# Optimization experiments

Measured on AMD Instinct MI355X. Metric: run time of the kernel, lower is better.

Reference implementation:

```python
import jax, jax.numpy as jnp
import numpy as np

# Problem sizes (see shape_source): 32 point clouds of 2048 points each.
B, P, K = 32, 2048, 20
DIN, H, OUT = 3, 128, 128
N = B * P
EPS = 1e-5  # BatchNorm eps (eval mode: running stats mean=0, var=1)


def setup_inputs() -> dict:
    key = jax.random.key(0)
    ks = jax.random.split(key, 8)
    x = jax.random.normal(ks[0], (N, DIN), dtype=jnp.float32)
    batch = (jnp.arange(N) // P).astype(jnp.int32)  # equal-size clouds

    def lin(k, i, o):
        return (jax.random.normal(k, (i, o), dtype=jnp.float32) / np.sqrt(i)).astype(jnp.float32)

    return {
        "x": x, "batch": batch,
        # transfer = MLP([input_dim, hid_dim]) -> single Linear
        "Wt": lin(ks[1], DIN, H), "bt": jnp.zeros((H,), jnp.float32),
        # GINConv layer 0: Linear(H,2H) -> ReLU -> Linear(2H,H)
        "W1_0": lin(ks[2], H, 2 * H), "b1_0": jnp.zeros((2 * H,), jnp.float32),
        "W2_0": lin(ks[3], 2 * H, H), "b2_0": jnp.zeros((H,), jnp.float32),
        "g0": jnp.ones((H,), jnp.float32), "be0": jnp.zeros((H,), jnp.float32),
        "rm0": jnp.zeros((H,), jnp.float32), "rv0": jnp.ones((H,), jnp.float32),
        # GINConv layer 1
        "W1_1": lin(ks[4], H, 2 * H), "b1_1": jnp.zeros((2 * H,), jnp.float32),
        "W2_1": lin(ks[5], 2 * H, OUT), "b2_1": jnp.zeros((OUT,), jnp.float32),
        "g1": jnp.ones((OUT,), jnp.float32), "be1": jnp.zeros((OUT,), jnp.float32),
        "rm1": jnp.zeros((OUT,), jnp.float32), "rv1": jnp.ones((OUT,), jnp.float32),
    }


def _knn_idx(x):
    """Per-cloud kNN (includes self, dist 0), returns global neighbor ids [N,K]."""
    xb = x.reshape(B, P, DIN)
    sq = jnp.sum(xb * xb, axis=-1)  # [B,P]
    # squared euclidean distance [B,P,P]
    dist = sq[:, :, None] + sq[:, None, :] - 2.0 * jnp.einsum('bpd,bqd->bpq', xb, xb)
    _, idx = jax.lax.top_k(-dist, K)  # [B,P,K] nearest (incl. self)
    offs = (jnp.arange(B, dtype=idx.dtype) * P)[:, None, None]
    return (idx + offs).reshape(N, K)


def _bn_eval(h, g, be, rm, rv):
    return g * (h - rm) * jax.lax.rsqrt(rv + EPS) + be


def _gin_max(h, nbr, W1, b1, W2, b2):
    # max-aggregation over kNN neighbors + self loop, then GIN MLP
    agg = jnp.maximum(jnp.max(h[nbr], axis=1), h)  # [N,d]
    return jax.nn.relu(agg @ W1 + b1) @ W2 + b2


def reference(x, batch, Wt, bt,
              W1_0, b1_0, W2_0, b2_0, g0, be0, rm0, rv0,
              W1_1, b1_1, W2_1, b2_1, g1, be1, rm1, rv1):
    nbr = _knn_idx(jax.lax.stop_gradient(x))  # knn(x, x, k, batch).flip([0])
    h = x @ Wt + bt  # transfer MLP (single Linear)
    # layer 0: GINConv(max) -> BN -> ReLU (dropout identity in eval)
    h = _gin_max(h, nbr, W1_0, b1_0, W2_0, b2_0)
    h = jax.nn.relu(_bn_eval(h, g0, be0, rm0, rv0))
    # layer 1 (last): GINConv(max) -> BN -> dropout (identity)
    h = _gin_max(h, nbr, W1_1, b1_1, W2_1, b2_1)
    h = _bn_eval(h, g1, be1, rm1, rv1)
    return h
```

## Files before the change

### kernel.cpp

```cpp
#include <hip/hip_runtime.h>

typedef unsigned int u32;
typedef unsigned short u16;
typedef unsigned long long u64;

#define NPTS 65536
#define PCLD 2048
#define KNN 20
#define HD 128
#define HD2 256

typedef __attribute__((ext_vector_type(8))) short bf16x8;
typedef __attribute__((ext_vector_type(4))) float f32x4;
typedef unsigned short us2 __attribute__((ext_vector_type(2)));

__device__ __forceinline__ u16 f2bf(float f) {
    u32 u = __float_as_uint(f);
    u32 r = (u + 0x7FFFu + ((u >> 16) & 1u)) >> 16;
    return (u16)r;
}
__device__ __forceinline__ u32 enc2(u32 b) {
    u32 s = (b >> 15) & 0x00010001u;
    return b ^ (s * 0x7FFFu) ^ 0x80008000u;
}
__device__ __forceinline__ u32 dec2(u32 e) {
    u32 s = ((~e) >> 15) & 0x00010001u;
    return e ^ (s * 0x7FFFu) ^ 0x80008000u;
}
__device__ __forceinline__ u32 max2(u32 a, u32 b) {
#if __has_builtin(__builtin_elementwise_max)
    us2 x, y; __builtin_memcpy(&x, &a, 4); __builtin_memcpy(&y, &b, 4);
    us2 r = __builtin_elementwise_max(x, y);
    u32 o; __builtin_memcpy(&o, &r, 4); return o;
#else
    u32 lo = ((a & 0xFFFFu) > (b & 0xFFFFu)) ? (a & 0xFFFFu) : (b & 0xFFFFu);
    u32 hi = ((a >> 16) > (b >> 16)) ? (a & 0xFFFF0000u) : (b & 0xFFFF0000u);
    return lo | hi;
#endif
}

__global__ __launch_bounds__(256) void prep_kernel(
    const float* __restrict__ W1_0, const float* __restrict__ W2_0,
    const float* __restrict__ W1_1, const float* __restrict__ W2_1,
    u16* __restrict__ W1_0T, u16* __restrict__ W2_0T,
    u16* __restrict__ W1_1T, u16* __restrict__ W2_1T) {
    int id = blockIdx.x * 256 + threadIdx.x;
    int m = id >> 15, e = id & 32767;
    if (m == 0)      { int n = e >> 7, k = e & 127; W1_0T[e] = f2bf(W1_0[k * 256 + n]); }
    else if (m == 1) { int n = e >> 8, k = e & 255; W2_0T[e] = f2bf(W2_0[k * 128 + n]); }
    else if (m == 2) { int n = e >> 7, k = e & 127; W1_1T[e] = f2bf(W1_1[k * 256 + n]); }
    else             { int n = e >> 8, k = e & 255; W2_1T[e] = f2bf(W2_1[k * 128 + n]); }
}

__global__ __launch_bounds__(256) void knn_kernel(const float* __restrict__ x,
                                                  u16* __restrict__ nbr) {
    __shared__ float4 pts[PCLD];
    const int cloud = blockIdx.x >> 3;
    const int qi = ((blockIdx.x & 7) << 8) + threadIdx.x;
    const float* xc = x + (u64)cloud * PCLD * 3;
    for (int t = threadIdx.x; t < PCLD; t += 256) {
        float a = xc[3 * t], b = xc[3 * t + 1], c = xc[3 * t + 2];
        float sq = __fadd_rn(__fadd_rn(__fmul_rn(a, a), __fmul_rn(b, b)), __fmul_rn(c, c));
        pts[t] = make_float4(a, b, c, sq);
    }
    __syncthreads();
    const float4 q = pts[qi];
    const float qx = q.x, qy = q.y, qz = q.z, qs = q.w;
    const int lane = threadIdx.x & 63;
    u64 list[KNN];
#pragma unroll
    for (int k = 0; k < KNN; ++k) list[k] = 0xFF800000FFFFFFFFull;
    float thr = __builtin_inff();

    for (int base = 0; base < PCLD; base += 64) {
        float4 cp = pts[base + lane];
        u64 mask = 0;
#pragma unroll
        for (int c = 0; c < 64; ++c) {
            float cx = __uint_as_float(__builtin_amdgcn_readlane(__float_as_uint(cp.x), c));
            float cy = __uint_as_float(__builtin_amdgcn_readlane(__float_as_uint(cp.y), c));
            float cz = __uint_as_float(__builtin_amdgcn_readlane(__float_as_uint(cp.z), c));
            float cs = __uint_as_float(__builtin_amdgcn_readlane(__float_as_uint(cp.w), c));
            float dot = __builtin_fmaf(cz, qz, __builtin_fmaf(cy, qy, __fmul_rn(cx, qx)));
            float d = __fsub_rn(__fadd_rn(qs, cs), __fmul_rn(2.0f, dot));
            if (d < thr) mask |= (1ull << c);
        }
        while (mask) {
            int c = __builtin_ctzll(mask);
            mask &= mask - 1;
            float4 p2 = pts[base + c];
            float dot = __builtin_fmaf(p2.z, qz, __builtin_fmaf(p2.y, qy, __fmul_rn(p2.x, qx)));
            float d = __fsub_rn(__fadd_rn(qs, p2.w), __fmul_rn(2.0f, dot));
            if (d < thr) {
                u32 ub = __float_as_uint(d);
                u32 e = (ub & 0x80000000u) ? ~ub : (ub | 0x80000000u);
                u64 key = (((u64)e) << 32) | (u32)(base + c);
#pragma unroll
                for (int k = 0; k < KNN; ++k) {
                    u64 lo = key < list[k] ? key : list[k];
                    u64 hi = key < list[k] ? list[k] : key;
                    list[k] = lo; key = hi;
                }
                u32 e19 = (u32)(list[KNN - 1] >> 32);
                u32 ud = (e19 & 0x80000000u) ? (e19 & 0x7FFFFFFFu) : ~e19;
                thr = __uint_as_float(ud);
            }
        }
    }
    u16* out = nbr + (u64)(cloud * PCLD + qi) * KNN;
#pragma unroll
    for (int k = 0; k < KNN; ++k) out[k] = (u16)(u32)list[k];
}

__global__ __launch_bounds__(256) void feat_kernel(const float* __restrict__ x,
                                                   const float* __restrict__ Wt,
                                                   const float* __restrict__ bt,
                                                   u16* __restrict__ h0e) {
    int gid = blockIdx.x * 256 + threadIdx.x;
    int i = gid >> 4;
    int g = gid & 15;
    int c0 = g << 3;
    float x0 = x[3 * i], x1 = x[3 * i + 1], x2 = x[3 * i + 2];
    u32 o[4];
#pragma unroll
    for (int j = 0; j < 8; j += 2) {
        int c = c0 + j;
        float a0 = bt[c]     + x0 * Wt[c]     + x1 * Wt[128 + c]     + x2 * Wt[256 + c];
        float a1 = bt[c + 1] + x0 * Wt[c + 1] + x1 * Wt[128 + c + 1] + x2 * Wt[256 + c + 1];
        o[j >> 1] = enc2(((u32)f2bf(a0)) | (((u32)f2bf(a1)) << 16));
    }
    uint4* dst = (uint4*)&h0e[(u64)g * NPTS * 8 + (u64)i * 8];
    *dst = make_uint4(o[0], o[1], o[2], o[3]);
}

__global__ __launch_bounds__(256) void agg_kernel(const u16* __restrict__ he,
                                                  const u16* __restrict__ nbr,
                                                  u16* __restrict__ agge) {
    __shared__ u16 hL[PCLD * 8];
    const int tid = threadIdx.x;
    const int cloud = blockIdx.x >> 4;
    const int s = blockIdx.x & 15;
    const u16* __restrict__ src = he + (u64)s * NPTS * 8 + (u64)cloud * PCLD * 8;

    for (int k = 0; k < 8; ++k) {
        int r = tid + 256 * k;
        *(uint4*)&hL[r * 8] = *(const uint4*)&src[(u64)r * 8];
    }
    __syncthreads();

    const int rowbase = cloud * PCLD;
    for (int k = 0; k < 8; ++k) {
        int r = tid + 256 * k;
        uint4 m = *(const uint4*)&hL[r * 8];
        const u64* nb8 = (const u64*)(nbr + (u64)(rowbase + r) * KNN);
        u64 nq[5];
#pragma unroll
        for (int w = 0; w < 5; ++w) nq[w] = nb8[w];
#pragma unroll
        for (int t = 0; t < KNN; ++t) {
            int loc = (int)(nq[t >> 2] >> ((t & 3) * 16)) & (PCLD - 1);
            uint4 v = *(const uint4*)&hL[loc * 8];
            m.x = max2(m.x, v.x); m.y = max2(m.y, v.y);
            m.z = max2(m.z, v.z); m.w = max2(m.w, v.w);
        }
        *(uint4*)&agge[(u64)s * NPTS * 8 + (u64)(rowbase + r) * 8] = m;
    }
}

template <int RELU_OUT, int OUT_F32>
__global__ __launch_bounds__(256) void gemm_kernel(
    const u16* __restrict__ agge,
    const u16* __restrict__ W1T, const float* __restrict__ b1,
    const u16* __restrict__ W2T, const float* __restrict__ b2,
    const float* __restrict__ g, const float* __restrict__ be,
    const float* __restrict__ rm, const float* __restrict__ rv,
    void* __restrict__ hout_v) {
    __shared__ u16 aggL[64][136];
    __shared__ u16 hidL[64][264];
    const int tid = threadIdx.x;
    const int R = blockIdx.x * 64;

    {
        const int r = tid >> 2, cg = tid & 3;
        const int gr = R + r;
#pragma unroll
        for (int h = 0; h < 4; ++h) {
            const int s = 4 * cg + h;
            const u32* src = (const u32*)(agge + (u64)s * NPTS * 8 + (u64)gr * 8);
            u32 w0 = src[0], w1 = src[1], w2 = src[2], w3 = src[3];
            u32* dst = (u32*)&aggL[r][cg * 32 + h * 8];
            dst[0] = dec2(w0); dst[1] = dec2(w1); dst[2] = dec2(w2); dst[3] = dec2(w3);
        }
    }
    __syncthreads();

    const int wv = tid >> 6, lane = tid & 63;
    const int lr = lane & 15;
    const int lq = lane >> 4;

    {
        f32x4 acc[4][4];
#pragma unroll
        for (int i = 0; i < 4; ++i)
#pragma unroll
            for (int j = 0; j < 4; ++j) acc[i][j] = (f32x4)(0.0f);
        const int nb0 = wv * 64;
#pragma unroll
        for (int ks = 0; ks < 4; ++ks) {
            const int kcol = ks * 32 + lq * 8;
            bf16x8 af[4], bfr[4];
#pragma unroll
            for (int mt = 0; mt < 4; ++mt)
                af[mt] = *(const bf16x8*)&aggL[mt * 16 + lr][kcol];
#pragma unroll
            for (int nt = 0; nt < 4; ++nt)
                bfr[nt] = *(const bf16x8*)&W1T[(u64)(nb0 + nt * 16 + lr) * HD + kcol];
#pragma unroll
            for (int mt = 0; mt < 4; ++mt)
#pragma unroll
                for (int nt = 0; nt < 4; ++nt)
                    acc[mt][nt] = __builtin_amdgcn_mfma_f32_16x16x32_bf16(af[mt], bfr[nt], acc[mt][nt], 0, 0, 0);
        }
#pragma unroll
        for (int nt = 0; nt < 4; ++nt) {
            const int c = nb0 + nt * 16 + lr;
            const float bias = b1[c];
#pragma unroll
            for (int mt = 0; mt < 4; ++mt)
#pragma unroll
                for (int r2 = 0; r2 < 4; ++r2) {
                    float v = fmaxf(acc[mt][nt][r2] + bias, 0.0f);
                    hidL[mt * 16 + lq * 4 + r2][c] = f2bf(v);
                }
        }
    }
    __syncthreads();

    {
        f32x4 acc[4][2];
#pragma unroll
        for (int i = 0; i < 4; ++i) { acc[i][0] = (f32x4)(0.0f); acc[i][1] = (f32x4)(0.0f); }
        const int nb0 = wv * 32;
#pragma unroll
        for (int ks = 0; ks < 8; ++ks) {
            const int kcol = ks * 32 + lq * 8;
            bf16x8 af[4], bfr[2];
#pragma unroll
            for (int mt = 0; mt < 4; ++mt)
                af[mt] = *(const bf16x8*)&hidL[mt * 16 + lr][kcol];
#pragma unroll
            for (int nt = 0; nt < 2; ++nt)
                bfr[nt] = *(const bf16x8*)&W2T[(u64)(nb0 + nt * 16 + lr) * HD2 + kcol];
#pragma unroll
            for (int mt = 0; mt < 4; ++mt)
#pragma unroll
                for (int nt = 0; nt < 2; ++nt)
                    acc[mt][nt] = __builtin_amdgcn_mfma_f32_16x16x32_bf16(af[mt], bfr[nt], acc[mt][nt], 0, 0, 0);
        }
#pragma unroll
        for (int nt = 0; nt < 2; ++nt) {
            const int c = nb0 + nt * 16 + lr;
            const float bias = b2[c];
            const float sc = g[c] * (1.0f / sqrtf(rv[c] + 1e-5f));
            const float rmc = rm[c];
            const float bec = be[c];
#pragma unroll
            for (int mt = 0; mt < 4; ++mt)
#pragma unroll
                for (int r2 = 0; r2 < 4; ++r2) {
                    float v = acc[mt][nt][r2] + bias;
                    v = (v - rmc) * sc + bec;
                    if (RELU_OUT) v = fmaxf(v, 0.0f);
                    const int row = R + mt * 16 + lq * 4 + r2;
                    if (OUT_F32) {
                        ((float*)hout_v)[(u64)row * HD + c] = v;
                    } else {
                        u16 b = f2bf(v);
                        u16 e = b ^ ((b & 0x8000u) ? (u16)0xFFFFu : (u16)0x8000u);
                        ((u16*)hout_v)[(u64)(c >> 3) * NPTS * 8 + (u64)row * 8 + (c & 7)] = e;
                    }
                }
        }
    }
}

extern "C" void kernel_launch(void* const* d_in, const int* in_sizes, int n_in,
                              void* d_out, int out_size, void* d_ws, size_t ws_size,
                              hipStream_t stream) {
    const float* x    = (const float*)d_in[0];
    const float* Wt   = (const float*)d_in[2];
    const float* bt   = (const float*)d_in[3];
    const float* W1_0 = (const float*)d_in[4];
    const float* b1_0 = (const float*)d_in[5];
    const float* W2_0 = (const float*)d_in[6];
    const float* b2_0 = (const float*)d_in[7];
    const float* g0   = (const float*)d_in[8];
    const float* be0  = (const float*)d_in[9];
    const float* rm0  = (const float*)d_in[10];
    const float* rv0  = (const float*)d_in[11];
    const float* W1_1 = (const float*)d_in[12];
    const float* b1_1 = (const float*)d_in[13];
    const float* W2_1 = (const float*)d_in[14];
    const float* b2_1 = (const float*)d_in[15];
    const float* g1   = (const float*)d_in[16];
    const float* be1  = (const float*)d_in[17];
    const float* rm1  = (const float*)d_in[18];
    const float* rv1  = (const float*)d_in[19];

    char* ws = (char*)d_ws;
    u16* he   = (u16*)ws;
    u16* agge = (u16*)(ws + 16777216);
    u16* W10T = (u16*)(ws + 2 * 16777216);
    u16* W20T = W10T + 32768;
    u16* W11T = W20T + 32768;
    u16* W21T = W11T + 32768;
    u16* nbr  = (u16*)(ws + 2 * 16777216 + 4 * 65536);

    knn_kernel<<<256, 256, 0, stream>>>(x, nbr);
    prep_kernel<<<512, 256, 0, stream>>>(W1_0, W2_0, W1_1, W2_1, W10T, W20T, W11T, W21T);
    feat_kernel<<<4096, 256, 0, stream>>>(x, Wt, bt, he);
    agg_kernel<<<512, 256, 0, stream>>>(he, nbr, agge);
    gemm_kernel<1, 0><<<1024, 256, 0, stream>>>(agge, W10T, b1_0, W20T, b2_0,
                                                g0, be0, rm0, rv0, he);
    agg_kernel<<<512, 256, 0, stream>>>(he, nbr, agge);
    gemm_kernel<0, 1><<<1024, 256, 0, stream>>>(agge, W11T, b1_1, W21T, b2_1,
                                                g1, be1, rm1, rv1, d_out);
}
```

Baseline: 344.2 us.

## Split kNN candidate scan across two thread halves and merge top-k lists

The kNN kernel now runs 512 threads per block. Each query is handled by two threads, and each thread scans half of the cloud's candidate points. The second half writes its sorted top-20 list to shared memory, and the first half merges it into its own list with an insertion network before writing the result. This doubles the number of active waves to expose more parallelism, since only 256 blocks were launched before. The cost is extra shared memory, a block barrier, a serial merge step, and weaker early thresholds in each half.

```diff
diff --git a/kernel.cpp b/kernel.cpp
--- a/kernel.cpp
+++ b/kernel.cpp
@@ -52,27 +52,31 @@
     else             { int n = e >> 8, k = e & 255; W2_1T[e] = f2bf(W2_1[k * 128 + n]); }
 }
 
-__global__ __launch_bounds__(256) void knn_kernel(const float* __restrict__ x,
+__global__ __launch_bounds__(512) void knn_kernel(const float* __restrict__ x,
                                                   u16* __restrict__ nbr) {
     __shared__ float4 pts[PCLD];
+    __shared__ u64 lists[KNN][256];
+    const int tid = threadIdx.x;
     const int cloud = blockIdx.x >> 3;
-    const int qi = ((blockIdx.x & 7) << 8) + threadIdx.x;
+    const int ql = ((blockIdx.x & 7) << 8) + (tid & 255);
+    const int half = tid >> 8;
     const float* xc = x + (u64)cloud * PCLD * 3;
-    for (int t = threadIdx.x; t < PCLD; t += 256) {
+    for (int t = tid; t < PCLD; t += 512) {
         float a = xc[3 * t], b = xc[3 * t + 1], c = xc[3 * t + 2];
         float sq = __fadd_rn(__fadd_rn(__fmul_rn(a, a), __fmul_rn(b, b)), __fmul_rn(c, c));
         pts[t] = make_float4(a, b, c, sq);
     }
     __syncthreads();
-    const float4 q = pts[qi];
+    const float4 q = pts[ql];
     const float qx = q.x, qy = q.y, qz = q.z, qs = q.w;
-    const int lane = threadIdx.x & 63;
+    const int lane = tid & 63;
     u64 list[KNN];
 #pragma unroll
     for (int k = 0; k < KNN; ++k) list[k] = 0xFF800000FFFFFFFFull;
     float thr = __builtin_inff();
 
-    for (int base = 0; base < PCLD; base += 64) {
+    const int cbeg = half << 10;
+    for (int base = cbeg; base < cbeg + 1024; base += 64) {
         float4 cp = pts[base + lane];
         u64 mask = 0;
 #pragma unroll
@@ -107,9 +111,27 @@
             }
         }
     }
-    u16* out = nbr + (u64)(cloud * PCLD + qi) * KNN;
-#pragma unroll
-    for (int k = 0; k < KNN; ++k) out[k] = (u16)(u32)list[k];
+
+    if (half) {
+#pragma unroll
+        for (int k = 0; k < KNN; ++k) lists[k][tid & 255] = list[k];
+    }
+    __syncthreads();
+    if (!half) {
+#pragma unroll
+        for (int j = 0; j < KNN; ++j) {
+            u64 key = lists[j][tid];
+#pragma unroll
+            for (int k = 0; k < KNN; ++k) {
+                u64 lo = key < list[k] ? key : list[k];
+                u64 hi = key < list[k] ? list[k] : key;
+                list[k] = lo; key = hi;
+            }
+        }
+        u16* out = nbr + (u64)(cloud * PCLD + ql) * KNN;
+#pragma unroll
+        for (int k = 0; k < KNN; ++k) out[k] = (u16)(u32)list[k];
+    }
 }
 
 __global__ __launch_bounds__(256) void feat_kernel(const float* __restrict__ x,
@@ -316,7 +338,7 @@
     u16* W21T = W11T + 32768;
     u16* nbr  = (u16*)(ws + 2 * 16777216 + 4 * 65536);
 
-    knn_kernel<<<256, 256, 0, stream>>>(x, nbr);
+    knn_kernel<<<256, 512, 0, stream>>>(x, nbr);
     prep_kernel<<<512, 256, 0, stream>>>(W1_0, W2_0, W1_1, W2_1, W10T, W20T, W11T, W21T);
     feat_kernel<<<4096, 256, 0, stream>>>(x, Wt, bt, he);
     agg_kernel<<<512, 256, 0, stream>>>(he, nbr, agge);
```

Measured after the change: 399.1 us. 1.16x slower.

## Fuse neighbor max-aggregation into GEMM kernel with row-major features

Applied to the files above, without the earlier changes.

Removes the separate LDS-based aggregation kernel and performs the kNN max-gather directly inside the GEMM kernel's tile load, reading neighbor rows from global memory in a row-major feature layout. Blocks are remapped so tiles of the same cloud land on the same XCD, aiming for L2 reuse of the cloud's features. This eliminates the agge round-trip and two launches, but replaces LDS gathers with scattered global gathers of 64-byte row chunks.

```diff
diff --git a/kernel.cpp b/kernel.cpp
--- a/kernel.cpp
+++ b/kernel.cpp
@@ -129,47 +129,13 @@
         float a1 = bt[c + 1] + x0 * Wt[c + 1] + x1 * Wt[128 + c + 1] + x2 * Wt[256 + c + 1];
         o[j >> 1] = enc2(((u32)f2bf(a0)) | (((u32)f2bf(a1)) << 16));
     }
-    uint4* dst = (uint4*)&h0e[(u64)g * NPTS * 8 + (u64)i * 8];
+    uint4* dst = (uint4*)&h0e[(u64)i * HD + c0];
     *dst = make_uint4(o[0], o[1], o[2], o[3]);
-}
-
-__global__ __launch_bounds__(256) void agg_kernel(const u16* __restrict__ he,
-                                                  const u16* __restrict__ nbr,
-                                                  u16* __restrict__ agge) {
-    __shared__ u16 hL[PCLD * 8];
-    const int tid = threadIdx.x;
-    const int cloud = blockIdx.x >> 4;
-    const int s = blockIdx.x & 15;
-    const u16* __restrict__ src = he + (u64)s * NPTS * 8 + (u64)cloud * PCLD * 8;
-
-    for (int k = 0; k < 8; ++k) {
-        int r = tid + 256 * k;
-        *(uint4*)&hL[r * 8] = *(const uint4*)&src[(u64)r * 8];
-    }
-    __syncthreads();
-
-    const int rowbase = cloud * PCLD;
-    for (int k = 0; k < 8; ++k) {
-        int r = tid + 256 * k;
-        uint4 m = *(const uint4*)&hL[r * 8];
-        const u64* nb8 = (const u64*)(nbr + (u64)(rowbase + r) * KNN);
-        u64 nq[5];
-#pragma unroll
-        for (int w = 0; w < 5; ++w) nq[w] = nb8[w];
-#pragma unroll
-        for (int t = 0; t < KNN; ++t) {
-            int loc = (int)(nq[t >> 2] >> ((t & 3) * 16)) & (PCLD - 1);
-            uint4 v = *(const uint4*)&hL[loc * 8];
-            m.x = max2(m.x, v.x); m.y = max2(m.y, v.y);
-            m.z = max2(m.z, v.z); m.w = max2(m.w, v.w);
-        }
-        *(uint4*)&agge[(u64)s * NPTS * 8 + (u64)(rowbase + r) * 8] = m;
-    }
 }
 
 template <int RELU_OUT, int OUT_F32>
 __global__ __launch_bounds__(256) void gemm_kernel(
-    const u16* __restrict__ agge,
+    const u16* __restrict__ he, const u16* __restrict__ nbr_,
     const u16* __restrict__ W1T, const float* __restrict__ b1,
     const u16* __restrict__ W2T, const float* __restrict__ b2,
     const float* __restrict__ g, const float* __restrict__ be,
@@ -178,19 +144,44 @@
     __shared__ u16 aggL[64][136];
     __shared__ u16 hidL[64][264];
     const int tid = threadIdx.x;
-    const int R = blockIdx.x * 64;
+    const int b = blockIdx.x;
+    const int xcd = b & 7, j = b >> 3;
+    const int cloud = xcd + 8 * (j >> 5);
+    const int tile = j & 31;
+    const int R = cloud * PCLD + tile * 64;
 
     {
         const int r = tid >> 2, cg = tid & 3;
-        const int gr = R + r;
-#pragma unroll
-        for (int h = 0; h < 4; ++h) {
-            const int s = 4 * cg + h;
-            const u32* src = (const u32*)(agge + (u64)s * NPTS * 8 + (u64)gr * 8);
-            u32 w0 = src[0], w1 = src[1], w2 = src[2], w3 = src[3];
-            u32* dst = (u32*)&aggL[r][cg * 32 + h * 8];
-            dst[0] = dec2(w0); dst[1] = dec2(w1); dst[2] = dec2(w2); dst[3] = dec2(w3);
-        }
+        const int grow = R + r;
+        const u16* __restrict__ hrow = he + (u64)grow * HD + cg * 32;
+        uint4 m0 = ((const uint4*)hrow)[0];
+        uint4 m1 = ((const uint4*)hrow)[1];
+        uint4 m2 = ((const uint4*)hrow)[2];
+        uint4 m3 = ((const uint4*)hrow)[3];
+        const u64* nb8 = (const u64*)(nbr_ + (u64)grow * KNN);
+        u64 nq[5];
+#pragma unroll
+        for (int w = 0; w < 5; ++w) nq[w] = nb8[w];
+        const u16* __restrict__ hcl = he + (u64)cloud * PCLD * HD + cg * 32;
+#pragma unroll 4
+        for (int t = 0; t < KNN; ++t) {
+            int loc = (int)(nq[t >> 2] >> ((t & 3) * 16)) & (PCLD - 1);
+            const uint4* vp = (const uint4*)(hcl + (u64)loc * HD);
+            uint4 v0 = vp[0], v1 = vp[1], v2 = vp[2], v3 = vp[3];
+            m0.x = max2(m0.x, v0.x); m0.y = max2(m0.y, v0.y);
+            m0.z = max2(m0.z, v0.z); m0.w = max2(m0.w, v0.w);
+            m1.x = max2(m1.x, v1.x); m1.y = max2(m1.y, v1.y);
+            m1.z = max2(m1.z, v1.z); m1.w = max2(m1.w, v1.w);
+            m2.x = max2(m2.x, v2.x); m2.y = max2(m2.y, v2.y);
+            m2.z = max2(m2.z, v2.z); m2.w = max2(m2.w, v2.w);
+            m3.x = max2(m3.x, v3.x); m3.y = max2(m3.y, v3.y);
+            m3.z = max2(m3.z, v3.z); m3.w = max2(m3.w, v3.w);
+        }
+        u32* dst = (u32*)&aggL[r][cg * 32];
+        dst[0] = dec2(m0.x); dst[1] = dec2(m0.y); dst[2] = dec2(m0.z); dst[3] = dec2(m0.w);
+        dst[4] = dec2(m1.x); dst[5] = dec2(m1.y); dst[6] = dec2(m1.z); dst[7] = dec2(m1.w);
+        dst[8] = dec2(m2.x); dst[9] = dec2(m2.y); dst[10] = dec2(m2.z); dst[11] = dec2(m2.w);
+        dst[12] = dec2(m3.x); dst[13] = dec2(m3.y); dst[14] = dec2(m3.z); dst[15] = dec2(m3.w);
     }
     __syncthreads();
 
@@ -203,7 +194,7 @@
 #pragma unroll
         for (int i = 0; i < 4; ++i)
 #pragma unroll
-            for (int j = 0; j < 4; ++j) acc[i][j] = (f32x4)(0.0f);
+            for (int j2 = 0; j2 < 4; ++j2) acc[i][j2] = (f32x4)(0.0f);
         const int nb0 = wv * 64;
 #pragma unroll
         for (int ks = 0; ks < 4; ++ks) {
@@ -275,9 +266,9 @@
                     if (OUT_F32) {
                         ((float*)hout_v)[(u64)row * HD + c] = v;
                     } else {
-                        u16 b = f2bf(v);
-                        u16 e = b ^ ((b & 0x8000u) ? (u16)0xFFFFu : (u16)0x8000u);
-                        ((u16*)hout_v)[(u64)(c >> 3) * NPTS * 8 + (u64)row * 8 + (c & 7)] = e;
+                        u16 bb = f2bf(v);
+                        u16 e = bb ^ ((bb & 0x8000u) ? (u16)0xFFFFu : (u16)0x8000u);
+                        ((u16*)hout_v)[(u64)row * HD + c] = e;
                     }
                 }
         }
@@ -308,8 +299,8 @@
     const float* rv1  = (const float*)d_in[19];
 
     char* ws = (char*)d_ws;
-    u16* he   = (u16*)ws;
-    u16* agge = (u16*)(ws + 16777216);
+    u16* he0  = (u16*)ws;
+    u16* he1  = (u16*)(ws + 16777216);
     u16* W10T = (u16*)(ws + 2 * 16777216);
     u16* W20T = W10T + 32768;
     u16* W11T = W20T + 32768;
@@ -318,11 +309,9 @@
 
     knn_kernel<<<256, 256, 0, stream>>>(x, nbr);
     prep_kernel<<<512, 256, 0, stream>>>(W1_0, W2_0, W1_1, W2_1, W10T, W20T, W11T, W21T);
-    feat_kernel<<<4096, 256, 0, stream>>>(x, Wt, bt, he);
-    agg_kernel<<<512, 256, 0, stream>>>(he, nbr, agge);
-    gemm_kernel<1, 0><<<1024, 256, 0, stream>>>(agge, W10T, b1_0, W20T, b2_0,
-                                                g0, be0, rm0, rv0, he);
-    agg_kernel<<<512, 256, 0, stream>>>(he, nbr, agge);
-    gemm_kernel<0, 1><<<1024, 256, 0, stream>>>(agge, W11T, b1_1, W21T, b2_1,
+    feat_kernel<<<4096, 256, 0, stream>>>(x, Wt, bt, he0);
+    gemm_kernel<1, 0><<<1024, 256, 0, stream>>>(he0, nbr, W10T, b1_0, W20T, b2_0,
+                                                g0, be0, rm0, rv0, he1);
+    gemm_kernel<0, 1><<<1024, 256, 0, stream>>>(he1, nbr, W11T, b1_1, W21T, b2_1,
                                                 g1, be1, rm1, rv1, d_out);
 }
```

Measured after the change: 340.4 us. No clear change (-1.1%).
